# Performance work log

Measured on AMD Instinct MI355X. Metric: run time of the kernel, lower is better.

The kernel has to match this reference:

```python
import jax, jax.numpy as jnp
import numpy as np

BN_EPS = 1e-5
LEAKY_SLOPE = 0.01

N_TOTAL, FEAT_DIM = 100000, 128
N_BATCH, K = 50000, 16
EMBED_DIM = 128


def setup_inputs() -> dict:
    key = jax.random.key(0)
    k1, k2, k3 = jax.random.split(key, 3)
    raw_features = jax.random.normal(k1, (N_TOTAL, FEAT_DIM), dtype=jnp.float32)
    weight = jax.random.normal(k2, (FEAT_DIM, EMBED_DIM), dtype=jnp.float32) * (1.0 / np.sqrt(FEAT_DIM))
    gamma = jnp.ones((EMBED_DIM,), dtype=jnp.float32)
    beta = jnp.zeros((EMBED_DIM,), dtype=jnp.float32)
    neigh_idx = jax.random.randint(k3, (N_BATCH, K), 0, N_TOTAL, dtype=jnp.int64)
    return {"raw_features": raw_features, "weight": weight, "gamma": gamma,
            "beta": beta, "neigh_idx": neigh_idx}


def reference(raw_features, weight, gamma, beta, neigh_idx):
    # Mean aggregation over sampled neighbors: [N_BATCH, K, F] -> [N_BATCH, F]
    neigh_feats = jnp.mean(raw_features[neigh_idx], axis=1)
    # Dense transform: [N_BATCH, EMBED_DIM]
    x = neigh_feats @ weight
    # BatchNorm1d (training mode: batch statistics, biased variance)
    mean = jnp.mean(x, axis=0)
    var = jnp.var(x, axis=0)
    x = (x - mean) * jax.lax.rsqrt(var + BN_EPS) * gamma + beta
    # LeakyReLU (default negative_slope=0.01)
    return jnp.where(x >= 0, x, LEAKY_SLOPE * x)
```

## Files before the change

kernel.cpp:

```cpp
#include <hip/hip_runtime.h>
#include <hip/hip_bf16.h>


#define NTOTAL 100000
#define FEAT   128
#define NB     50000
#define KNEI   16
#define NTILES (NB / 16)
#define ZTILES (NTOTAL / 16)
#define NSLOT  8
#define NSTRIPE ((NB + 127) / 128)

#define OFF_PSTAT 0
#define OFF_ZC    8192
#define OFF_XB    (8192 + 25600000)
#define WS_NEEDED (OFF_XB + 12800000)

typedef float f32x4 __attribute__((ext_vector_type(4)));
typedef short bf16x8 __attribute__((ext_vector_type(8)));
typedef int   i32x4 __attribute__((ext_vector_type(4)));

__device__ __forceinline__ unsigned short f2bf(float f) {
    union { float f; unsigned u; } v; v.f = f;
    unsigned r = v.u + 0x7FFF + ((v.u >> 16) & 1);
    return (unsigned short)(r >> 16);
}

#define WT_LD 136
#define A_LD  136
#define SLAB_ELEMS ((size_t)NTOTAL * 16)

__global__ __launch_bounds__(256, 4) void enc_zgemm(
    const float* __restrict__ raw, const float* __restrict__ W,
    unsigned short* __restrict__ Zc, float* __restrict__ pstats)
{
    __shared__ unsigned short sWt[128 * WT_LD];
    __shared__ unsigned short sA[16 * A_LD];

    const int t = threadIdx.x;

    if (blockIdx.x == 0) {
        #pragma unroll
        for (int i = 0; i < NSLOT; ++i) pstats[t + i * 256] = 0.f;
    }

    #pragma unroll
    for (int i = 0; i < 16; ++i) {
        int e = t + i * 256;
        float4 w4 = ((const float4*)W)[e];
        int li = e * 4;
        int k = li >> 7, n = li & 127;
        sWt[(n + 0) * WT_LD + k] = f2bf(w4.x);
        sWt[(n + 1) * WT_LD + k] = f2bf(w4.y);
        sWt[(n + 2) * WT_LD + k] = f2bf(w4.z);
        sWt[(n + 3) * WT_LD + k] = f2bf(w4.w);
    }

    const int lane = t & 63;
    const int wv = t >> 6;
    const int ln = lane & 15;
    const int qd = lane >> 4;
    const int c2 = t & 15;
    const int g  = t >> 4;
    const int n0 = wv * 32 + ln, n1 = n0 + 16;
    const int s0 = wv * 2, s1 = wv * 2 + 1;

    for (int tile = blockIdx.x; tile < ZTILES; tile += gridDim.x) {
        const int r0 = tile * 16;
        __syncthreads();
        {
            const float4* rp = (const float4*)&raw[(size_t)(r0 + g) * FEAT + c2 * 8];
            float4 x0 = rp[0], x1 = rp[1];
            uint4 b;
            b.x = (unsigned)f2bf(x0.x) | ((unsigned)f2bf(x0.y) << 16);
            b.y = (unsigned)f2bf(x0.z) | ((unsigned)f2bf(x0.w) << 16);
            b.z = (unsigned)f2bf(x1.x) | ((unsigned)f2bf(x1.y) << 16);
            b.w = (unsigned)f2bf(x1.z) | ((unsigned)f2bf(x1.w) << 16);
            *(uint4*)&sA[g * A_LD + c2 * 8] = b;
        }
        __syncthreads();

        f32x4 acc0 = {0.f, 0.f, 0.f, 0.f}, acc1 = {0.f, 0.f, 0.f, 0.f};
        #pragma unroll
        for (int kt = 0; kt < 4; ++kt) {
            const int k0 = kt * 32 + qd * 8;
            bf16x8 a  = *(const bf16x8*)&sA[ln * A_LD + k0];
            bf16x8 b0 = *(const bf16x8*)&sWt[n0 * WT_LD + k0];
            bf16x8 b1 = *(const bf16x8*)&sWt[n1 * WT_LD + k0];
            acc0 = __builtin_amdgcn_mfma_f32_16x16x32_bf16(a, b0, acc0, 0, 0, 0);
            acc1 = __builtin_amdgcn_mfma_f32_16x16x32_bf16(a, b1, acc1, 0, 0, 0);
        }

        #pragma unroll
        for (int ri = 0; ri < 4; ++ri) {
            const int row = r0 + qd * 4 + ri;
            Zc[(size_t)s0 * SLAB_ELEMS + (size_t)row * 16 + ln] = f2bf(acc0[ri]);
            Zc[(size_t)s1 * SLAB_ELEMS + (size_t)row * 16 + ln] = f2bf(acc1[ri]);
        }
    }
}

__global__ __launch_bounds__(256, 4) void enc_gather_slab(
    const unsigned short* __restrict__ Zc, const int* __restrict__ idx,
    unsigned short* __restrict__ xb, float* __restrict__ pstats)
{
    __shared__ int sidx[2048];
    __shared__ float sRed[128];

    const int t = threadIdx.x;
    const int fc = blockIdx.x & 7;
    const int stripe = blockIdx.x >> 3;
    const int r0 = stripe * 128;

    {
        const int base = r0 * KNEI + t * 8;
        if (base + 7 < NB * KNEI) {
            const i32x4* g4 = (const i32x4*)&idx[base];
            i32x4 v0 = __builtin_nontemporal_load(&g4[0]);
            i32x4 v1 = __builtin_nontemporal_load(&g4[1]);
            *(i32x4*)&sidx[t * 8]     = v0;
            *(i32x4*)&sidx[t * 8 + 4] = v1;
        }
    }
    __syncthreads();

    const int r = t >> 1;
    const int h = t & 1;
    const int row = r0 + r;
    const bool valid = row < NB;

    const unsigned short* slab = Zc + (size_t)fc * SLAB_ELEMS;

    float a[8];
    #pragma unroll
    for (int j = 0; j < 8; ++j) a[j] = 0.f;

    if (valid) {
        const int* ip = &sidx[r * KNEI];
        uint4 v[16];
        #pragma unroll
        for (int k = 0; k < KNEI; ++k)
            v[k] = *(const uint4*)&slab[(size_t)ip[k] * 16 + h * 8];
        __builtin_amdgcn_sched_barrier(0);
        #pragma unroll
        for (int k = 0; k < KNEI; ++k) {
            a[0] += __uint_as_float(v[k].x << 16);
            a[1] += __uint_as_float(v[k].x & 0xFFFF0000u);
            a[2] += __uint_as_float(v[k].y << 16);
            a[3] += __uint_as_float(v[k].y & 0xFFFF0000u);
            a[4] += __uint_as_float(v[k].z << 16);
            a[5] += __uint_as_float(v[k].z & 0xFFFF0000u);
            a[6] += __uint_as_float(v[k].w << 16);
            a[7] += __uint_as_float(v[k].w & 0xFFFF0000u);
        }
        #pragma unroll
        for (int j = 0; j < 8; ++j) a[j] *= 0.0625f;

        uint4 b;
        b.x = (unsigned)f2bf(a[0]) | ((unsigned)f2bf(a[1]) << 16);
        b.y = (unsigned)f2bf(a[2]) | ((unsigned)f2bf(a[3]) << 16);
        b.z = (unsigned)f2bf(a[4]) | ((unsigned)f2bf(a[5]) << 16);
        b.w = (unsigned)f2bf(a[6]) | ((unsigned)f2bf(a[7]) << 16);
        *(uint4*)&xb[(size_t)row * FEAT + fc * 16 + h * 8] = b;
    }

    float q[8];
    #pragma unroll
    for (int j = 0; j < 8; ++j) q[j] = a[j] * a[j];
    #pragma unroll
    for (int j = 0; j < 8; ++j) {
        a[j] += __shfl_down(a[j], 32); q[j] += __shfl_down(q[j], 32);
        a[j] += __shfl_down(a[j], 16); q[j] += __shfl_down(q[j], 16);
        a[j] += __shfl_down(a[j], 8);  q[j] += __shfl_down(q[j], 8);
        a[j] += __shfl_down(a[j], 4);  q[j] += __shfl_down(q[j], 4);
        a[j] += __shfl_down(a[j], 2);  q[j] += __shfl_down(q[j], 2);
    }
    const int lane = t & 63, wv = t >> 6;
    if (lane < 2) {
        #pragma unroll
        for (int j = 0; j < 8; ++j) {
            sRed[wv * 16 + h * 8 + j]      = a[j];
            sRed[64 + wv * 16 + h * 8 + j] = q[j];
        }
    }
    __syncthreads();
    if (t < 16) {
        float u1 = sRed[t] + sRed[16 + t] + sRed[32 + t] + sRed[48 + t];
        float u2 = sRed[64 + t] + sRed[80 + t] + sRed[96 + t] + sRed[112 + t];
        const int slot = stripe & (NSLOT - 1);
        atomicAdd(&pstats[slot * 256 + fc * 16 + t], u1);
        atomicAdd(&pstats[slot * 256 + 128 + fc * 16 + t], u2);
    }
}

__global__ __launch_bounds__(256) void enc_bn(
    const unsigned short* __restrict__ xb, float* __restrict__ out,
    const float* __restrict__ pstats,
    const float* __restrict__ gamma, const float* __restrict__ beta)
{
    __shared__ float sScale[FEAT], sShift[FEAT];
    const int t = threadIdx.x;
    if (t < FEAT) {
        float s1 = 0.f, s2 = 0.f;
        #pragma unroll
        for (int sl = 0; sl < NSLOT; ++sl) {
            s1 += pstats[sl * 256 + t];
            s2 += pstats[sl * 256 + 128 + t];
        }
        float mean = s1 * (1.0f / NB);
        float var = s2 * (1.0f / NB) - mean * mean;
        float sc = gamma[t] * rsqrtf(var + 1e-5f);
        sScale[t] = sc;
        sShift[t] = beta[t] - mean * sc;
    }
    __syncthreads();

    const int f8 = (t & 15) * 8;
    const float4 sc0 = *(const float4*)&sScale[f8], sc1 = *(const float4*)&sScale[f8 + 4];
    const float4 sh0 = *(const float4*)&sShift[f8], sh1 = *(const float4*)&sShift[f8 + 4];

    const uint4* x4 = (const uint4*)xb;
    float4* o4 = (float4*)out;
    const int total8 = NB * FEAT / 8;
    for (int e = blockIdx.x * 256 + t; e < total8; e += gridDim.x * 256) {
        uint4 v = x4[e];
        float4 r0, r1; float y;
        y = __uint_as_float(v.x << 16)        * sc0.x + sh0.x; r0.x = (y >= 0.f) ? y : 0.01f * y;
        y = __uint_as_float(v.x & 0xFFFF0000u)* sc0.y + sh0.y; r0.y = (y >= 0.f) ? y : 0.01f * y;
        y = __uint_as_float(v.y << 16)        * sc0.z + sh0.z; r0.z = (y >= 0.f) ? y : 0.01f * y;
        y = __uint_as_float(v.y & 0xFFFF0000u)* sc0.w + sh0.w; r0.w = (y >= 0.f) ? y : 0.01f * y;
        y = __uint_as_float(v.z << 16)        * sc1.x + sh1.x; r1.x = (y >= 0.f) ? y : 0.01f * y;
        y = __uint_as_float(v.z & 0xFFFF0000u)* sc1.y + sh1.y; r1.y = (y >= 0.f) ? y : 0.01f * y;
        y = __uint_as_float(v.w << 16)        * sc1.z + sh1.z; r1.z = (y >= 0.f) ? y : 0.01f * y;
        y = __uint_as_float(v.w & 0xFFFF0000u)* sc1.w + sh1.w; r1.w = (y >= 0.f) ? y : 0.01f * y;
        o4[e * 2] = r0; o4[e * 2 + 1] = r1;
    }
}

__global__ __launch_bounds__(256, 4) void enc_gemm_f(
    const float* __restrict__ raw, const float* __restrict__ W,
    const int* __restrict__ idx, float* __restrict__ out,
    float* __restrict__ gstats)
{
    __shared__ unsigned short sWt[128 * WT_LD];
    __shared__ unsigned short sA[16 * A_LD];
    __shared__ int sidx[256];
    const int t = threadIdx.x;
    #pragma unroll 4
    for (int i = 0; i < 64; ++i) {
        int e = t + i * 256;
        int f = e >> 7, n = e & 127;
        sWt[n * WT_LD + f] = f2bf(W[e]);
    }
    const int lane = t & 63, wv = t >> 6, ln = lane & 15, qd = lane >> 4;
    const int c = t & 31, g = t >> 5;
    const int n0 = wv * 32 + ln, n1 = n0 + 16;
    float s1a = 0.f, s2a = 0.f, s1b = 0.f, s2b = 0.f;
    const float4* raw4 = (const float4*)raw;
    for (int tile = blockIdx.x; tile < NTILES; tile += gridDim.x) {
        const int i0 = tile * 16;
        __syncthreads();
        sidx[t] = idx[i0 * KNEI + t];
        __syncthreads();
        #pragma unroll
        for (int rr = 0; rr < 2; ++rr) {
            const int r = g * 2 + rr;
            const int* ip = &sidx[r * KNEI];
            float4 acc = {0.f, 0.f, 0.f, 0.f};
            #pragma unroll
            for (int k = 0; k < KNEI; ++k) {
                float4 v = raw4[(size_t)ip[k] * 32 + c];
                acc.x += v.x; acc.y += v.y; acc.z += v.z; acc.w += v.w;
            }
            ushort4 b;
            b.x = f2bf(acc.x * 0.0625f); b.y = f2bf(acc.y * 0.0625f);
            b.z = f2bf(acc.z * 0.0625f); b.w = f2bf(acc.w * 0.0625f);
            *(ushort4*)&sA[r * A_LD + c * 4] = b;
        }
        __syncthreads();
        f32x4 acc0 = {0.f, 0.f, 0.f, 0.f}, acc1 = {0.f, 0.f, 0.f, 0.f};
        #pragma unroll
        for (int kt = 0; kt < 4; ++kt) {
            const int k0 = kt * 32 + qd * 8;
            bf16x8 a  = *(const bf16x8*)&sA[ln * A_LD + k0];
            bf16x8 b0 = *(const bf16x8*)&sWt[n0 * WT_LD + k0];
            bf16x8 b1 = *(const bf16x8*)&sWt[n1 * WT_LD + k0];
            acc0 = __builtin_amdgcn_mfma_f32_16x16x32_bf16(a, b0, acc0, 0, 0, 0);
            acc1 = __builtin_amdgcn_mfma_f32_16x16x32_bf16(a, b1, acc1, 0, 0, 0);
        }
        #pragma unroll
        for (int ri = 0; ri < 4; ++ri) {
            const int row = i0 + qd * 4 + ri;
            float v0 = acc0[ri], v1 = acc1[ri];
            out[row * FEAT + n0] = v0;
            out[row * FEAT + n1] = v1;
            s1a += v0; s2a += v0 * v0;
            s1b += v1; s2b += v1 * v1;
        }
    }
    s1a += __shfl_down(s1a, 32); s1a += __shfl_down(s1a, 16);
    s2a += __shfl_down(s2a, 32); s2a += __shfl_down(s2a, 16);
    s1b += __shfl_down(s1b, 32); s1b += __shfl_down(s1b, 16);
    s2b += __shfl_down(s2b, 32); s2b += __shfl_down(s2b, 16);
    if (qd == 0) {
        atomicAdd(&gstats[n0], s1a);
        atomicAdd(&gstats[FEAT + n0], s2a);
        atomicAdd(&gstats[n1], s1b);
        atomicAdd(&gstats[FEAT + n1], s2b);
    }
}

__global__ __launch_bounds__(256) void enc_bn_f(
    float* __restrict__ out, const float* __restrict__ gstats,
    const float* __restrict__ gamma, const float* __restrict__ beta)
{
    __shared__ float sScale[FEAT], sShift[FEAT];
    const int t = threadIdx.x;
    if (t < FEAT) {
        float s1 = gstats[t], s2 = gstats[FEAT + t];
        float mean = s1 * (1.0f / NB);
        float var = s2 * (1.0f / NB) - mean * mean;
        float sc = gamma[t] * rsqrtf(var + 1e-5f);
        sScale[t] = sc;
        sShift[t] = beta[t] - mean * sc;
    }
    __syncthreads();
    const int f4 = (t & 31) * 4;
    const float4 sc = *(const float4*)&sScale[f4];
    const float4 sh = *(const float4*)&sShift[f4];
    const int total4 = NB * FEAT / 4;
    float4* o4 = (float4*)out;
    for (int e = blockIdx.x * 256 + t; e < total4; e += gridDim.x * 256) {
        float4 v = o4[e];
        float4 r; float y;
        y = v.x * sc.x + sh.x; r.x = (y >= 0.f) ? y : 0.01f * y;
        y = v.y * sc.y + sh.y; r.y = (y >= 0.f) ? y : 0.01f * y;
        y = v.z * sc.z + sh.z; r.z = (y >= 0.f) ? y : 0.01f * y;
        y = v.w * sc.w + sh.w; r.w = (y >= 0.f) ? y : 0.01f * y;
        o4[e] = r;
    }
}

extern "C" void kernel_launch(void* const* d_in, const int* in_sizes, int n_in,
                              void* d_out, int out_size, void* d_ws, size_t ws_size,
                              hipStream_t stream) {
    const float* raw   = (const float*)d_in[0];
    const float* W     = (const float*)d_in[1];
    const float* gamma = (const float*)d_in[2];
    const float* beta  = (const float*)d_in[3];
    const int*   idx   = (const int*)d_in[4];
    float* out = (float*)d_out;

    char* ws = (char*)d_ws;

    if (ws_size >= WS_NEEDED) {
        float* pstats      = (float*)(ws + OFF_PSTAT);
        unsigned short* Zc = (unsigned short*)(ws + OFF_ZC);
        unsigned short* xb = (unsigned short*)(ws + OFF_XB);
        enc_zgemm<<<1042, 256, 0, stream>>>(raw, W, Zc, pstats);
        enc_gather_slab<<<NSTRIPE * 8, 256, 0, stream>>>(Zc, idx, xb, pstats);
        enc_bn<<<1024, 256, 0, stream>>>(xb, out, pstats, gamma, beta);
    } else {
        float* gstats = (float*)(ws + OFF_PSTAT);
        (void)hipMemsetAsync(gstats, 0, 2 * FEAT * sizeof(float), stream);
        enc_gemm_f<<<1024, 256, 0, stream>>>(raw, W, idx, out, gstats);
        enc_bn_f<<<1024, 256, 0, stream>>>(out, gstats, gamma, beta);
    }
}
```

Before: 164.7 us.

## Split neighbor gather across four lanes per row with 1024-thread blocks

After: 180.5 us. 1.1x slower.

```diff
diff --git a/kernel.cpp b/kernel.cpp
--- a/kernel.cpp
+++ b/kernel.cpp
@@ -100,12 +100,12 @@
     }
 }
 
-__global__ __launch_bounds__(256, 4) void enc_gather_slab(
+__global__ __launch_bounds__(1024, 2) void enc_gather_slab4(
     const unsigned short* __restrict__ Zc, const int* __restrict__ idx,
     unsigned short* __restrict__ xb, float* __restrict__ pstats)
 {
     __shared__ int sidx[2048];
-    __shared__ float sRed[128];
+    __shared__ float sRed[2 * 16 * 16];
 
     const int t = threadIdx.x;
     const int fc = blockIdx.x & 7;
@@ -113,19 +113,19 @@
     const int r0 = stripe * 128;
 
     {
-        const int base = r0 * KNEI + t * 8;
-        if (base + 7 < NB * KNEI) {
-            const i32x4* g4 = (const i32x4*)&idx[base];
-            i32x4 v0 = __builtin_nontemporal_load(&g4[0]);
-            i32x4 v1 = __builtin_nontemporal_load(&g4[1]);
-            *(i32x4*)&sidx[t * 8]     = v0;
-            *(i32x4*)&sidx[t * 8 + 4] = v1;
-        }
+        int o0 = r0 * KNEI + t;
+        if (o0 < NB * KNEI) sidx[t] = __builtin_nontemporal_load(&idx[o0]);
+        int o1 = o0 + 1024;
+        if (o1 < NB * KNEI) sidx[t + 1024] = __builtin_nontemporal_load(&idx[o1]);
     }
     __syncthreads();
 
-    const int r = t >> 1;
-    const int h = t & 1;
+    const int lane = t & 63;
+    const int w  = t >> 6;
+    const int rl = lane >> 3;
+    const int kg = (lane >> 1) & 3;
+    const int h  = lane & 1;
+    const int r  = w * 8 + rl;
     const int row = r0 + r;
     const bool valid = row < NB;
 
@@ -136,26 +136,33 @@
     for (int j = 0; j < 8; ++j) a[j] = 0.f;
 
     if (valid) {
-        const int* ip = &sidx[r * KNEI];
-        uint4 v[16];
-        #pragma unroll
-        for (int k = 0; k < KNEI; ++k)
-            v[k] = *(const uint4*)&slab[(size_t)ip[k] * 16 + h * 8];
+        const int* ip = &sidx[r * KNEI + kg * 4];
+        uint4 v[4];
+        #pragma unroll
+        for (int kk = 0; kk < 4; ++kk)
+            v[kk] = *(const uint4*)&slab[(size_t)ip[kk] * 16 + h * 8];
         __builtin_amdgcn_sched_barrier(0);
         #pragma unroll
-        for (int k = 0; k < KNEI; ++k) {
-            a[0] += __uint_as_float(v[k].x << 16);
-            a[1] += __uint_as_float(v[k].x & 0xFFFF0000u);
-            a[2] += __uint_as_float(v[k].y << 16);
-            a[3] += __uint_as_float(v[k].y & 0xFFFF0000u);
-            a[4] += __uint_as_float(v[k].z << 16);
-            a[5] += __uint_as_float(v[k].z & 0xFFFF0000u);
-            a[6] += __uint_as_float(v[k].w << 16);
-            a[7] += __uint_as_float(v[k].w & 0xFFFF0000u);
-        }
-        #pragma unroll
-        for (int j = 0; j < 8; ++j) a[j] *= 0.0625f;
-
+        for (int kk = 0; kk < 4; ++kk) {
+            a[0] += __uint_as_float(v[kk].x << 16);
+            a[1] += __uint_as_float(v[kk].x & 0xFFFF0000u);
+            a[2] += __uint_as_float(v[kk].y << 16);
+            a[3] += __uint_as_float(v[kk].y & 0xFFFF0000u);
+            a[4] += __uint_as_float(v[kk].z << 16);
+            a[5] += __uint_as_float(v[kk].z & 0xFFFF0000u);
+            a[6] += __uint_as_float(v[kk].w << 16);
+            a[7] += __uint_as_float(v[kk].w & 0xFFFF0000u);
+        }
+    }
+
+    #pragma unroll
+    for (int j = 0; j < 8; ++j) {
+        a[j] += __shfl_down(a[j], 4);
+        a[j] += __shfl_down(a[j], 2);
+        a[j] *= 0.0625f;
+    }
+
+    if (((lane & 6) == 0) && valid) {
         uint4 b;
         b.x = (unsigned)f2bf(a[0]) | ((unsigned)f2bf(a[1]) << 16);
         b.y = (unsigned)f2bf(a[2]) | ((unsigned)f2bf(a[3]) << 16);
@@ -172,21 +179,22 @@
         a[j] += __shfl_down(a[j], 32); q[j] += __shfl_down(q[j], 32);
         a[j] += __shfl_down(a[j], 16); q[j] += __shfl_down(q[j], 16);
         a[j] += __shfl_down(a[j], 8);  q[j] += __shfl_down(q[j], 8);
-        a[j] += __shfl_down(a[j], 4);  q[j] += __shfl_down(q[j], 4);
-        a[j] += __shfl_down(a[j], 2);  q[j] += __shfl_down(q[j], 2);
-    }
-    const int lane = t & 63, wv = t >> 6;
+    }
     if (lane < 2) {
         #pragma unroll
         for (int j = 0; j < 8; ++j) {
-            sRed[wv * 16 + h * 8 + j]      = a[j];
-            sRed[64 + wv * 16 + h * 8 + j] = q[j];
+            sRed[w * 16 + h * 8 + j]       = a[j];
+            sRed[256 + w * 16 + h * 8 + j] = q[j];
         }
     }
     __syncthreads();
     if (t < 16) {
-        float u1 = sRed[t] + sRed[16 + t] + sRed[32 + t] + sRed[48 + t];
-        float u2 = sRed[64 + t] + sRed[80 + t] + sRed[96 + t] + sRed[112 + t];
+        float u1 = 0.f, u2 = 0.f;
+        #pragma unroll
+        for (int ww = 0; ww < 16; ++ww) {
+            u1 += sRed[ww * 16 + t];
+            u2 += sRed[256 + ww * 16 + t];
+        }
         const int slot = stripe & (NSLOT - 1);
         atomicAdd(&pstats[slot * 256 + fc * 16 + t], u1);
         atomicAdd(&pstats[slot * 256 + 128 + fc * 16 + t], u2);
@@ -358,7 +366,7 @@
         unsigned short* Zc = (unsigned short*)(ws + OFF_ZC);
         unsigned short* xb = (unsigned short*)(ws + OFF_XB);
         enc_zgemm<<<1042, 256, 0, stream>>>(raw, W, Zc, pstats);
-        enc_gather_slab<<<NSTRIPE * 8, 256, 0, stream>>>(Zc, idx, xb, pstats);
+        enc_gather_slab4<<<NSTRIPE * 8, 1024, 0, stream>>>(Zc, idx, xb, pstats);
         enc_bn<<<1024, 256, 0, stream>>>(xb, out, pstats, gamma, beta);
     } else {
         float* gstats = (float*)(ws + OFF_PSTAT);
```
